# Performance work log

Measured on AMD Instinct MI355X. Metric: run time of the kernel, lower is better.

## Reference

```python
import jax, jax.numpy as jnp
import numpy as np

SQ, B, H = 2048, 1, 4096
NP, HN, MQG = 32, 128, 2          # query heads, head_dim, kv groups
ROT = HN // 2                      # rotary dim = 64 (partial rotary)
NORM = float(np.sqrt(HN))


def apply_rope(x, rope):
    # x: [sq, b, nh, hn]; rope: [sq, 1, ROT//2, 2] (cos, sin)
    sq, b, nh, hn = x.shape
    rot = rope.shape[-2] * 2
    xr, xp = x[..., :rot], x[..., rot:]
    xs = xr.reshape(sq, b, nh, rot // 2, 2)
    rc = rope[:sq].reshape(sq, -1, 1, rot // 2, 2)
    o0 = xs[..., 0] * rc[..., 0] - xs[..., 1] * rc[..., 1]
    o1 = xs[..., 1] * rc[..., 0] + xs[..., 0] * rc[..., 1]
    out = jnp.stack([o0, o1], -1).reshape(sq, b, nh, rot)
    return jnp.concatenate([out, xp], axis=-1)


def setup_inputs() -> dict:
    key = jax.random.key(0)
    k0, k1, k2, k3 = jax.random.split(key, 4)
    qkv_dim = NP * HN + 2 * MQG * HN  # 4608
    hidden_states = jax.random.normal(k0, (SQ, B, H), jnp.float32) * 0.02
    Wqkv = jax.random.normal(k1, (qkv_dim, H), jnp.float32) * 0.02
    bqkv = jax.random.normal(k2, (qkv_dim,), jnp.float32) * 0.02
    Wdense = jax.random.normal(k3, (H, NP * HN), jnp.float32) * 0.02
    # rope cache [sq, 1, ROT//2, 2]
    pos = jnp.arange(SQ, dtype=jnp.float32)
    inv = 1.0 / (10000.0 ** (jnp.arange(0, ROT, 2, dtype=jnp.float32) / ROT))
    ang = pos[:, None] * inv[None, :]
    rotary_pos_emb = jnp.stack([jnp.cos(ang), jnp.sin(ang)], -1)[:, None, :, :]
    # additive causal mask [b, 1, sq, sq]
    causal = jnp.tril(jnp.ones((SQ, SQ), bool))
    attention_mask = jnp.broadcast_to(
        jnp.where(causal, 0.0, -1e9).astype(jnp.float32), (B, 1, SQ, SQ))
    return dict(hidden_states=hidden_states, Wqkv=Wqkv, bqkv=bqkv,
                Wdense=Wdense, rotary_pos_emb=rotary_pos_emb,
                attention_mask=attention_mask)


def reference(hidden_states, Wqkv, bqkv, Wdense, rotary_pos_emb, attention_mask):
    sq, b, _ = hidden_states.shape
    mixed = hidden_states @ Wqkv.T + bqkv            # [sq, b, 4608]
    qd, kvd = NP * HN, MQG * HN
    q = mixed[..., :qd].reshape(sq, b, NP, HN)
    k = mixed[..., qd:qd + kvd].reshape(sq, b, MQG, HN)
    v = mixed[..., qd + kvd:].reshape(sq, b, MQG, HN)
    q = apply_rope(q, rotary_pos_emb)
    k = apply_rope(k, rotary_pos_emb)
    # -> [b, heads, sq, hn]
    q = q.transpose(1, 2, 0, 3)
    k = k.transpose(1, 2, 0, 3)
    v = v.transpose(1, 2, 0, 3)
    # MQA grouping: q [b, g, n_rep, sq, hn]; kv kept at [b, g, sq, hn]
    n_rep = NP // MQG
    qg = q.reshape(b, MQG, n_rep, sq, HN)
    scores = jnp.einsum('bgrqd,bgkd->bgrqk', qg, k) / NORM
    scores = scores + attention_mask[:, None]        # [b,1,1,sq,sq] broadcast
    probs = jax.nn.softmax(scores.astype(jnp.float32), axis=-1).astype(q.dtype)
    ctx = jnp.einsum('bgrqk,bgkd->bgrqd', probs, v)  # [b, g, n_rep, sq, hn]
    ctx = ctx.reshape(b, NP, sq, HN).transpose(0, 2, 1, 3).reshape(b, sq, NP * HN)
    out = ctx @ Wdense.T                             # [b, sq, H]
    return out
```

## Files before the change

kernel.cpp:

```cpp
#include <hip/hip_runtime.h>
#include <stdint.h>

#define SQL 2048
#define HID 4096
#define NHEADS 32
#define HDSZ 128
#define QKVD 4608
#define QDIM 4096

typedef unsigned short u16;
typedef __attribute__((ext_vector_type(8))) short short8;
typedef __attribute__((ext_vector_type(4))) float f32x4;

#define AS1(p) ((__attribute__((address_space(1))) void*)(p))
#define AS3(p) ((__attribute__((address_space(3))) void*)(p))

__device__ __forceinline__ float bf2f(u16 u) {
  return __uint_as_float(((uint32_t)u) << 16);
}
__device__ __forceinline__ u16 f2bf(float f) {
  uint32_t x = __float_as_uint(f);
  x += 0x7fffu + ((x >> 16) & 1u);
  return (u16)(x >> 16);
}

__global__ void k_cvt(const float* __restrict__ in, u16* __restrict__ out, int n8) {
  int i = blockIdx.x * blockDim.x + threadIdx.x;
  int stride = gridDim.x * blockDim.x;
  for (; i < n8; i += stride) {
    const float4* p = reinterpret_cast<const float4*>(in) + (size_t)i * 2;
    float4 a = p[0], b = p[1];
    short8 o;
    o[0] = (short)f2bf(a.x); o[1] = (short)f2bf(a.y);
    o[2] = (short)f2bf(a.z); o[3] = (short)f2bf(a.w);
    o[4] = (short)f2bf(b.x); o[5] = (short)f2bf(b.y);
    o[6] = (short)f2bf(b.z); o[7] = (short)f2bf(b.w);
    reinterpret_cast<short8*>(out)[i] = o;
  }
}

template<int MODE>
__global__ __launch_bounds__(256, 2)
void k_gemm(const u16* __restrict__ A, const u16* __restrict__ B,
            const float* __restrict__ bias,
            u16* __restrict__ qbuf, u16* __restrict__ kbuf, u16* __restrict__ vtbuf,
            float* __restrict__ outf)
{
  __shared__ __align__(16) u16 ldsA[128 * 64];
  __shared__ __align__(16) u16 ldsB[128 * 64];
  const int tid = threadIdx.x;
  const int wid = tid >> 6, lane = tid & 63;
  const int l15 = lane & 15, lg = lane >> 4;
  const int m0 = blockIdx.y * 128, n0 = blockIdx.x * 128;
  const int wr = wid >> 1, wc = wid & 1;

  f32x4 acc[4][4] = {};

  const int srow = lane >> 3;
  const int skb  = (((lane & 7) ^ srow) << 4);
  const size_t rowbytes = (size_t)HID * 2;

  for (int t = 0; t < HID / 64; ++t) {
    __syncthreads();
    const char* Ab = (const char*)A + (size_t)m0 * rowbytes + (size_t)t * 128;
    const char* Bb = (const char*)B + (size_t)n0 * rowbytes + (size_t)t * 128;
#pragma unroll
    for (int i = 0; i < 4; ++i) {
      int seg = i * 4 + wid;
      int row = seg * 8 + srow;
      __builtin_amdgcn_global_load_lds(AS1(Ab + (size_t)row * rowbytes + skb),
                                       AS3(ldsA + seg * 512), 16, 0, 0);
      __builtin_amdgcn_global_load_lds(AS1(Bb + (size_t)row * rowbytes + skb),
                                       AS3(ldsB + seg * 512), 16, 0, 0);
    }
    __syncthreads();
#pragma unroll
    for (int kc = 0; kc < 2; ++kc) {
      short8 af[4], bfr[4];
#pragma unroll
      for (int mi = 0; mi < 4; ++mi) {
        int row = wr * 64 + mi * 16 + l15;
        int kb = (kc * 64 + lg * 16) ^ ((row & 7) << 4);
        af[mi] = *reinterpret_cast<const short8*>((const char*)ldsA + row * 128 + kb);
      }
#pragma unroll
      for (int ni = 0; ni < 4; ++ni) {
        int row = wc * 64 + ni * 16 + l15;
        int kb = (kc * 64 + lg * 16) ^ ((row & 7) << 4);
        bfr[ni] = *reinterpret_cast<const short8*>((const char*)ldsB + row * 128 + kb);
      }
#pragma unroll
      for (int mi = 0; mi < 4; ++mi)
#pragma unroll
        for (int ni = 0; ni < 4; ++ni)
          acc[mi][ni] = __builtin_amdgcn_mfma_f32_16x16x32_bf16(af[mi], bfr[ni], acc[mi][ni], 0, 0, 0);
    }
  }

#pragma unroll
  for (int mi = 0; mi < 4; ++mi) {
#pragma unroll
    for (int ni = 0; ni < 4; ++ni) {
      int row0 = m0 + wr * 64 + mi * 16 + lg * 4;
      int col  = n0 + wc * 64 + ni * 16 + l15;
      if (MODE == 0) {
        float bv = bias[col];
#pragma unroll
        for (int j = 0; j < 4; ++j) {
          float v = acc[mi][ni][j] + bv;
          u16 hb = f2bf(v);
          int r = row0 + j;
          if (col < QDIM) {
            int hh = col >> 7, d = col & 127;
            qbuf[((size_t)hh * SQL + r) * HDSZ + d] = hb;
          } else if (col < QDIM + 256) {
            int c2 = col - QDIM; int g = c2 >> 7, d = c2 & 127;
            kbuf[((size_t)g * SQL + r) * HDSZ + d] = hb;
          } else {
            int c2 = col - QDIM - 256; int g = c2 >> 7, d = c2 & 127;
            vtbuf[((size_t)g * HDSZ + d) * SQL + r] = hb;
          }
        }
      } else {
#pragma unroll
        for (int j = 0; j < 4; ++j)
          outf[(size_t)(row0 + j) * QDIM + col] = acc[mi][ni][j];
      }
    }
  }
}

__global__ void k_rope(u16* __restrict__ qbuf, u16* __restrict__ kbuf,
                       const float* __restrict__ rope) {
  int idx = blockIdx.x * blockDim.x + threadIdx.x;
  if (idx >= SQL * 34 * 32) return;
  int p = idx & 31;
  int hh = (idx >> 5) % 34;
  int s = idx / (34 * 32);
  float c  = rope[s * 64 + p * 2 + 0];
  float sn = rope[s * 64 + p * 2 + 1];
  u16* base = (hh < 32) ? (qbuf + ((size_t)hh * SQL + s) * HDSZ)
                        : (kbuf + ((size_t)(hh - 32) * SQL + s) * HDSZ);
  u16* pp = base + 2 * p;
  uint32_t packed = *reinterpret_cast<uint32_t*>(pp);
  float x0 = bf2f((u16)(packed & 0xffff));
  float x1 = bf2f((u16)(packed >> 16));
  float o0 = x0 * c - x1 * sn;
  float o1 = x1 * c + x0 * sn;
  *reinterpret_cast<uint32_t*>(pp) = (uint32_t)f2bf(o0) | ((uint32_t)f2bf(o1) << 16);
}

__global__ __launch_bounds__(64)
void k_attn(const u16* __restrict__ qbuf, const u16* __restrict__ kbuf,
            const u16* __restrict__ vtbuf, u16* __restrict__ ctx)
{
  __shared__ __align__(16) u16 pls[32 * 72];
  const int lane = threadIdx.x;
  const int l15 = lane & 15, lg = lane >> 4;
  const int h = blockIdx.x;
  const int g = h >> 4;
  const int qi = (int)gridDim.y - 1 - (int)blockIdx.y;
  const int q0 = qi * 32;
  const float inv_norm = 0.08838834764831845f;

  short8 aq[2][4];
#pragma unroll
  for (int rt = 0; rt < 2; ++rt) {
    const u16* qp = qbuf + ((size_t)h * SQL + q0 + rt * 16 + l15) * HDSZ + lg * 8;
#pragma unroll
    for (int kc = 0; kc < 4; ++kc)
      aq[rt][kc] = *reinterpret_cast<const short8*>(qp + kc * 32);
  }
  f32x4 o[2][8] = {};
  float mrow[2][4], lrow[2][4];
#pragma unroll
  for (int rt = 0; rt < 2; ++rt)
#pragma unroll
    for (int j = 0; j < 4; ++j) { mrow[rt][j] = -__builtin_inff(); lrow[rt][j] = 0.f; }

  const int jend = q0 + 31;
  for (int j0 = 0; j0 <= jend; j0 += 64) {
    short8 bk[4][4];
    const u16* kp = kbuf + ((size_t)g * SQL + j0 + l15) * HDSZ + lg * 8;
#pragma unroll
    for (int kt = 0; kt < 4; ++kt)
#pragma unroll
      for (int kc = 0; kc < 4; ++kc)
        bk[kt][kc] = *reinterpret_cast<const short8*>(kp + (size_t)kt * 16 * HDSZ + kc * 32);

    f32x4 s[2][4] = {};
    __builtin_amdgcn_s_setprio(1);
#pragma unroll
    for (int kc = 0; kc < 4; ++kc)
#pragma unroll
      for (int rt = 0; rt < 2; ++rt)
#pragma unroll
        for (int kt = 0; kt < 4; ++kt)
          s[rt][kt] = __builtin_amdgcn_mfma_f32_16x16x32_bf16(aq[rt][kc], bk[kt][kc], s[rt][kt], 0, 0, 0);
    __builtin_amdgcn_s_setprio(0);

    short8 bv[8][2];
    const u16* vp = vtbuf + ((size_t)g * HDSZ + l15) * SQL + j0 + lg * 8;
#pragma unroll
    for (int df = 0; df < 8; ++df)
#pragma unroll
      for (int kc2 = 0; kc2 < 2; ++kc2)
        bv[df][kc2] = *reinterpret_cast<const short8*>(vp + (size_t)df * 16 * SQL + kc2 * 32);

    float al[2][4];
#pragma unroll
    for (int rt = 0; rt < 2; ++rt) {
#pragma unroll
      for (int j = 0; j < 4; ++j) {
        int row = q0 + rt * 16 + lg * 4 + j;
        float v[4];
#pragma unroll
        for (int kt = 0; kt < 4; ++kt) {
          float sv = s[rt][kt][j] * inv_norm;
          v[kt] = (j0 + kt * 16 + l15 > row) ? -1e30f : sv;
        }
        float rm = fmaxf(fmaxf(v[0], v[1]), fmaxf(v[2], v[3]));
        rm = fmaxf(rm, __shfl_xor(rm, 1));
        rm = fmaxf(rm, __shfl_xor(rm, 2));
        rm = fmaxf(rm, __shfl_xor(rm, 4));
        rm = fmaxf(rm, __shfl_xor(rm, 8));
        float mn = fmaxf(mrow[rt][j], rm);
        float a = __expf(mrow[rt][j] - mn);
        mrow[rt][j] = mn;
        float p[4], ps = 0.f;
#pragma unroll
        for (int kt = 0; kt < 4; ++kt) { p[kt] = __expf(v[kt] - mn); ps += p[kt]; }
        ps += __shfl_xor(ps, 1);
        ps += __shfl_xor(ps, 2);
        ps += __shfl_xor(ps, 4);
        ps += __shfl_xor(ps, 8);
        lrow[rt][j] = lrow[rt][j] * a + ps;
        al[rt][j] = a;
        int rl = rt * 16 + lg * 4 + j;
#pragma unroll
        for (int kt = 0; kt < 4; ++kt)
          pls[rl * 72 + kt * 16 + l15] = f2bf(p[kt]);
      }
    }
    asm volatile("s_waitcnt lgkmcnt(0)" ::: "memory");

    short8 ap[2][2];
#pragma unroll
    for (int rt = 0; rt < 2; ++rt)
#pragma unroll
      for (int kc2 = 0; kc2 < 2; ++kc2)
        ap[rt][kc2] = *reinterpret_cast<const short8*>(&pls[(rt * 16 + l15) * 72 + kc2 * 32 + lg * 8]);

    __builtin_amdgcn_s_setprio(1);
#pragma unroll
    for (int rt = 0; rt < 2; ++rt) {
#pragma unroll
      for (int df = 0; df < 8; ++df) {
        f32x4 t = o[rt][df];
        t[0] *= al[rt][0]; t[1] *= al[rt][1]; t[2] *= al[rt][2]; t[3] *= al[rt][3];
        t = __builtin_amdgcn_mfma_f32_16x16x32_bf16(ap[rt][0], bv[df][0], t, 0, 0, 0);
        t = __builtin_amdgcn_mfma_f32_16x16x32_bf16(ap[rt][1], bv[df][1], t, 0, 0, 0);
        o[rt][df] = t;
      }
    }
    __builtin_amdgcn_s_setprio(0);
  }

#pragma unroll
  for (int rt = 0; rt < 2; ++rt) {
#pragma unroll
    for (int j = 0; j < 4; ++j) {
      float inv_l = 1.0f / lrow[rt][j];
      int row = q0 + rt * 16 + lg * 4 + j;
      u16* cp = ctx + (size_t)row * QDIM + h * HDSZ;
#pragma unroll
      for (int df = 0; df < 8; ++df)
        cp[df * 16 + l15] = f2bf(o[rt][df][j] * inv_l);
    }
  }
}


extern "C" void kernel_launch(void* const* d_in, const int* in_sizes, int n_in,
                              void* d_out, int out_size, void* d_ws, size_t ws_size,
                              hipStream_t stream) {
  const float* hs     = (const float*)d_in[0];
  const float* wqkv   = (const float*)d_in[1];
  const float* bqkv   = (const float*)d_in[2];
  const float* wdense = (const float*)d_in[3];
  const float* rope   = (const float*)d_in[4];
  char* ws = (char*)d_ws;
  u16* hid_b = (u16*)(ws + 0);
  u16* w_b   = (u16*)(ws + 16777216);
  u16* qb    = (u16*)(ws + 54525952);
  u16* kb    = (u16*)(ws + 71303168);
  u16* vtb   = (u16*)(ws + 72351744);
  u16* ctx   = hid_b;
  float* outf = (float*)d_out;

  k_cvt<<<2048, 256, 0, stream>>>(hs,   hid_b, SQL * HID / 8);
  k_cvt<<<2048, 256, 0, stream>>>(wqkv, w_b,   QKVD * HID / 8);
  k_gemm<0><<<dim3(QKVD / 128, SQL / 128), 256, 0, stream>>>(
      hid_b, w_b, bqkv, qb, kb, vtb, nullptr);
  k_rope<<<(SQL * 34 * 32) / 256, 256, 0, stream>>>(qb, kb, rope);
  k_cvt<<<2048, 256, 0, stream>>>(wdense, w_b, QDIM * HID / 8);
  k_attn<<<dim3(NHEADS, SQL / 32), 64, 0, stream>>>(qb, kb, vtb, ctx);
  k_gemm<1><<<dim3(QDIM / 128, SQL / 128), 256, 0, stream>>>(
      ctx, w_b, nullptr, nullptr, nullptr, nullptr, outf);
}
```

Before: 338.4 us.

## Split long causal attention rows across two KV chunks with a merge kernel

```diff
diff --git a/kernel.cpp b/kernel.cpp
--- a/kernel.cpp
+++ b/kernel.cpp
@@ -150,17 +150,32 @@
   *reinterpret_cast<uint32_t*>(pp) = (uint32_t)f2bf(o0) | ((uint32_t)f2bf(o1) << 16);
 }
 
+template<int SPLIT>
 __global__ __launch_bounds__(64)
 void k_attn(const u16* __restrict__ qbuf, const u16* __restrict__ kbuf,
-            const u16* __restrict__ vtbuf, u16* __restrict__ ctx)
+            const u16* __restrict__ vtbuf,
+            u16* __restrict__ part, float2* __restrict__ mlbuf,
+            u16* __restrict__ ctx)
 {
   __shared__ __align__(16) u16 pls[32 * 72];
   const int lane = threadIdx.x;
   const int l15 = lane & 15, lg = lane >> 4;
   const int h = blockIdx.x;
   const int g = h >> 4;
-  const int qi = (int)gridDim.y - 1 - (int)blockIdx.y;
+  int qi, ci;
+  if (SPLIT) {
+    int p = blockIdx.y;
+    if (p < 32)      { qi = 32 + p;  ci = 0; }
+    else if (p < 64) { qi = 95 - p;  ci = 1; }
+    else             { qi = 95 - p;  ci = 0; }
+  } else {
+    qi = (int)gridDim.y - 1 - (int)blockIdx.y;
+    ci = 0;
+  }
   const int q0 = qi * 32;
+  const int E  = q0 + 32;
+  const int c0 = SPLIT ? ci * 1024 : 0;
+  const int c1 = SPLIT ? min(c0 + 1024, E) : E;
   const float inv_norm = 0.08838834764831845f;
 
   short8 aq[2][4];
@@ -178,8 +193,7 @@
 #pragma unroll
     for (int j = 0; j < 4; ++j) { mrow[rt][j] = -__builtin_inff(); lrow[rt][j] = 0.f; }
 
-  const int jend = q0 + 31;
-  for (int j0 = 0; j0 <= jend; j0 += 64) {
+  for (int j0 = c0; j0 < c1; j0 += 64) {
     short8 bk[4][4];
     const u16* kp = kbuf + ((size_t)g * SQL + j0 + l15) * HDSZ + lg * 8;
 #pragma unroll
@@ -207,6 +221,7 @@
       for (int kc2 = 0; kc2 < 2; ++kc2)
         bv[df][kc2] = *reinterpret_cast<const short8*>(vp + (size_t)df * 16 * SQL + kc2 * 32);
 
+    const bool domask = (j0 + 63 > q0);
     float al[2][4];
 #pragma unroll
     for (int rt = 0; rt < 2; ++rt) {
@@ -214,10 +229,14 @@
       for (int j = 0; j < 4; ++j) {
         int row = q0 + rt * 16 + lg * 4 + j;
         float v[4];
-#pragma unroll
-        for (int kt = 0; kt < 4; ++kt) {
-          float sv = s[rt][kt][j] * inv_norm;
-          v[kt] = (j0 + kt * 16 + l15 > row) ? -1e30f : sv;
+        if (domask) {
+#pragma unroll
+          for (int kt = 0; kt < 4; ++kt)
+            v[kt] = (j0 + kt * 16 + l15 > row) ? -1e30f : s[rt][kt][j] * inv_norm;
+        } else {
+#pragma unroll
+          for (int kt = 0; kt < 4; ++kt)
+            v[kt] = s[rt][kt][j] * inv_norm;
         }
         float rm = fmaxf(fmaxf(v[0], v[1]), fmaxf(v[2], v[3]));
         rm = fmaxf(rm, __shfl_xor(rm, 1));
@@ -266,20 +285,72 @@
     __builtin_amdgcn_s_setprio(0);
   }
 
-#pragma unroll
-  for (int rt = 0; rt < 2; ++rt) {
-#pragma unroll
-    for (int j = 0; j < 4; ++j) {
-      float inv_l = 1.0f / lrow[rt][j];
-      int row = q0 + rt * 16 + lg * 4 + j;
-      u16* cp = ctx + (size_t)row * QDIM + h * HDSZ;
-#pragma unroll
-      for (int df = 0; df < 8; ++df)
-        cp[df * 16 + l15] = f2bf(o[rt][df][j] * inv_l);
-    }
-  }
-}
-
+  if (SPLIT) {
+    const int pid = (h * 64 + qi) * 2 + ci;
+    u16* pp = part + (size_t)pid * 32 * 128;
+#pragma unroll
+    for (int rt = 0; rt < 2; ++rt) {
+#pragma unroll
+      for (int j = 0; j < 4; ++j) {
+        float inv_l = 1.0f / lrow[rt][j];
+        int rl = rt * 16 + lg * 4 + j;
+#pragma unroll
+        for (int df = 0; df < 8; ++df)
+          pp[rl * 128 + df * 16 + l15] = f2bf(o[rt][df][j] * inv_l);
+        if (l15 == 0)
+          mlbuf[pid * 32 + rl] = make_float2(mrow[rt][j], lrow[rt][j]);
+      }
+    }
+  } else {
+#pragma unroll
+    for (int rt = 0; rt < 2; ++rt) {
+#pragma unroll
+      for (int j = 0; j < 4; ++j) {
+        float inv_l = 1.0f / lrow[rt][j];
+        int row = q0 + rt * 16 + lg * 4 + j;
+        u16* cp = ctx + (size_t)row * QDIM + h * HDSZ;
+#pragma unroll
+        for (int df = 0; df < 8; ++df)
+          cp[df * 16 + l15] = f2bf(o[rt][df][j] * inv_l);
+      }
+    }
+  }
+}
+
+__global__ __launch_bounds__(256)
+void k_merge(const u16* __restrict__ part, const float2* __restrict__ mlbuf,
+             u16* __restrict__ ctx)
+{
+  int idx = blockIdx.x * 256 + threadIdx.x;
+  int d8  = idx & 15;
+  int row = (idx >> 4) & 2047;
+  int h   = idx >> 15;
+  int qi = row >> 5, rl = row & 31;
+  int pid0 = (h * 64 + qi) * 2;
+  float2 ml0 = mlbuf[pid0 * 32 + rl];
+  short8 p0 = *reinterpret_cast<const short8*>(part + ((size_t)pid0 * 32 + rl) * 128 + d8 * 8);
+  short8 p1 = p0;
+  float w0 = ml0.y, w1 = 0.f;
+  if (qi >= 32) {
+    float2 ml1 = mlbuf[(pid0 + 1) * 32 + rl];
+    p1 = *reinterpret_cast<const short8*>(part + ((size_t)(pid0 + 1) * 32 + rl) * 128 + d8 * 8);
+    float ms = fmaxf(ml0.x, ml1.x);
+    w0 = ml0.y * __expf(ml0.x - ms);
+    w1 = ml1.y * __expf(ml1.x - ms);
+  }
+  float inv_s = 1.0f / (w0 + w1);
+  w0 *= inv_s; w1 *= inv_s;
+  short8 o;
+#pragma unroll
+  for (int e = 0; e < 8; ++e)
+    o[e] = (short)f2bf(w0 * bf2f((u16)p0[e]) + w1 * bf2f((u16)p1[e]));
+  *reinterpret_cast<short8*>(ctx + (size_t)row * QDIM + h * 128 + d8 * 8) = o;
+}
+
+
+#define WS_PART 73400320ull
+#define WS_ML   106954752ull
+#define WS_NEED 108003328ull
 
 extern "C" void kernel_launch(void* const* d_in, const int* in_sizes, int n_in,
                               void* d_out, int out_size, void* d_ws, size_t ws_size,
@@ -295,6 +366,8 @@
   u16* qb    = (u16*)(ws + 54525952);
   u16* kb    = (u16*)(ws + 71303168);
   u16* vtb   = (u16*)(ws + 72351744);
+  u16* part  = (u16*)(ws + WS_PART);
+  float2* ml = (float2*)(ws + WS_ML);
   u16* ctx   = hid_b;
   float* outf = (float*)d_out;
 
@@ -304,7 +377,12 @@
       hid_b, w_b, bqkv, qb, kb, vtb, nullptr);
   k_rope<<<(SQL * 34 * 32) / 256, 256, 0, stream>>>(qb, kb, rope);
   k_cvt<<<2048, 256, 0, stream>>>(wdense, w_b, QDIM * HID / 8);
-  k_attn<<<dim3(NHEADS, SQL / 32), 64, 0, stream>>>(qb, kb, vtb, ctx);
+  if (ws_size >= WS_NEED) {
+    k_attn<1><<<dim3(NHEADS, 96), 64, 0, stream>>>(qb, kb, vtb, part, ml, nullptr);
+    k_merge<<<(NHEADS * SQL * 16) / 256, 256, 0, stream>>>(part, ml, ctx);
+  } else {
+    k_attn<0><<<dim3(NHEADS, SQL / 32), 64, 0, stream>>>(qb, kb, vtb, nullptr, nullptr, ctx);
+  }
   k_gemm<1><<<dim3(QDIM / 128, SQL / 128), 256, 0, stream>>>(
       ctx, w_b, nullptr, nullptr, nullptr, nullptr, outf);
 }
```

Result: slower. 369.7 us (+9.3%).

## Transpose score MFMA, fold softmax scale into Q, and add lazy rescaling

Applied to the files above, without the earlier changes.

```diff
diff --git a/kernel.cpp b/kernel.cpp
--- a/kernel.cpp
+++ b/kernel.cpp
@@ -108,17 +108,17 @@
 #pragma unroll
         for (int j = 0; j < 4; ++j) {
           float v = acc[mi][ni][j] + bv;
-          u16 hb = f2bf(v);
           int r = row0 + j;
           if (col < QDIM) {
+            v *= 0.08838834764831845f;
             int hh = col >> 7, d = col & 127;
-            qbuf[((size_t)hh * SQL + r) * HDSZ + d] = hb;
+            qbuf[((size_t)hh * SQL + r) * HDSZ + d] = f2bf(v);
           } else if (col < QDIM + 256) {
             int c2 = col - QDIM; int g = c2 >> 7, d = c2 & 127;
-            kbuf[((size_t)g * SQL + r) * HDSZ + d] = hb;
+            kbuf[((size_t)g * SQL + r) * HDSZ + d] = f2bf(v);
           } else {
             int c2 = col - QDIM - 256; int g = c2 >> 7, d = c2 & 127;
-            vtbuf[((size_t)g * HDSZ + d) * SQL + r] = hb;
+            vtbuf[((size_t)g * HDSZ + d) * SQL + r] = f2bf(v);
           }
         }
       } else {
@@ -154,14 +154,13 @@
 void k_attn(const u16* __restrict__ qbuf, const u16* __restrict__ kbuf,
             const u16* __restrict__ vtbuf, u16* __restrict__ ctx)
 {
-  __shared__ __align__(16) u16 pls[32 * 72];
+  __shared__ uint32_t plw[32][36];
   const int lane = threadIdx.x;
   const int l15 = lane & 15, lg = lane >> 4;
   const int h = blockIdx.x;
   const int g = h >> 4;
   const int qi = (int)gridDim.y - 1 - (int)blockIdx.y;
   const int q0 = qi * 32;
-  const float inv_norm = 0.08838834764831845f;
 
   short8 aq[2][4];
 #pragma unroll
@@ -172,11 +171,9 @@
       aq[rt][kc] = *reinterpret_cast<const short8*>(qp + kc * 32);
   }
   f32x4 o[2][8] = {};
-  float mrow[2][4], lrow[2][4];
-#pragma unroll
-  for (int rt = 0; rt < 2; ++rt)
-#pragma unroll
-    for (int j = 0; j < 4; ++j) { mrow[rt][j] = -__builtin_inff(); lrow[rt][j] = 0.f; }
+  float mrow[2], lrow[2];
+#pragma unroll
+  for (int rt = 0; rt < 2; ++rt) { mrow[rt] = -__builtin_inff(); lrow[rt] = 0.f; }
 
   const int jend = q0 + 31;
   for (int j0 = 0; j0 <= jend; j0 += 64) {
@@ -188,7 +185,7 @@
       for (int kc = 0; kc < 4; ++kc)
         bk[kt][kc] = *reinterpret_cast<const short8*>(kp + (size_t)kt * 16 * HDSZ + kc * 32);
 
-    f32x4 s[2][4] = {};
+    f32x4 st[2][4] = {};
     __builtin_amdgcn_s_setprio(1);
 #pragma unroll
     for (int kc = 0; kc < 4; ++kc)
@@ -196,7 +193,7 @@
       for (int rt = 0; rt < 2; ++rt)
 #pragma unroll
         for (int kt = 0; kt < 4; ++kt)
-          s[rt][kt] = __builtin_amdgcn_mfma_f32_16x16x32_bf16(aq[rt][kc], bk[kt][kc], s[rt][kt], 0, 0, 0);
+          st[rt][kt] = __builtin_amdgcn_mfma_f32_16x16x32_bf16(bk[kt][kc], aq[rt][kc], st[rt][kt], 0, 0, 0);
     __builtin_amdgcn_s_setprio(0);
 
     short8 bv[8][2];
@@ -207,40 +204,62 @@
       for (int kc2 = 0; kc2 < 2; ++kc2)
         bv[df][kc2] = *reinterpret_cast<const short8*>(vp + (size_t)df * 16 * SQL + kc2 * 32);
 
-    float al[2][4];
+    const bool domask = (j0 + 63 > q0);
 #pragma unroll
     for (int rt = 0; rt < 2; ++rt) {
-#pragma unroll
-      for (int j = 0; j < 4; ++j) {
-        int row = q0 + rt * 16 + lg * 4 + j;
-        float v[4];
-#pragma unroll
-        for (int kt = 0; kt < 4; ++kt) {
-          float sv = s[rt][kt][j] * inv_norm;
-          v[kt] = (j0 + kt * 16 + l15 > row) ? -1e30f : sv;
-        }
-        float rm = fmaxf(fmaxf(v[0], v[1]), fmaxf(v[2], v[3]));
-        rm = fmaxf(rm, __shfl_xor(rm, 1));
-        rm = fmaxf(rm, __shfl_xor(rm, 2));
-        rm = fmaxf(rm, __shfl_xor(rm, 4));
-        rm = fmaxf(rm, __shfl_xor(rm, 8));
-        float mn = fmaxf(mrow[rt][j], rm);
-        float a = __expf(mrow[rt][j] - mn);
-        mrow[rt][j] = mn;
-        float p[4], ps = 0.f;
-#pragma unroll
-        for (int kt = 0; kt < 4; ++kt) { p[kt] = __expf(v[kt] - mn); ps += p[kt]; }
-        ps += __shfl_xor(ps, 1);
-        ps += __shfl_xor(ps, 2);
-        ps += __shfl_xor(ps, 4);
-        ps += __shfl_xor(ps, 8);
-        lrow[rt][j] = lrow[rt][j] * a + ps;
-        al[rt][j] = a;
-        int rl = rt * 16 + lg * 4 + j;
-#pragma unroll
-        for (int kt = 0; kt < 4; ++kt)
-          pls[rl * 72 + kt * 16 + l15] = f2bf(p[kt]);
-      }
+      const int q = q0 + rt * 16 + l15;
+      float p[4][4];
+#pragma unroll
+      for (int kt = 0; kt < 4; ++kt)
+#pragma unroll
+        for (int j = 0; j < 4; ++j) {
+          float v = st[rt][kt][j];
+          if (domask) {
+            int kvi = j0 + kt * 16 + lg * 4 + j;
+            v = (kvi > q) ? -1e30f : v;
+          }
+          p[kt][j] = v;
+        }
+      float rm = fmaxf(fmaxf(fmaxf(p[0][0], p[0][1]), fmaxf(p[0][2], p[0][3])),
+                       fmaxf(fmaxf(p[1][0], p[1][1]), fmaxf(p[1][2], p[1][3])));
+      rm = fmaxf(rm, fmaxf(fmaxf(fmaxf(p[2][0], p[2][1]), fmaxf(p[2][2], p[2][3])),
+                           fmaxf(fmaxf(p[3][0], p[3][1]), fmaxf(p[3][2], p[3][3]))));
+      rm = fmaxf(rm, __shfl_xor(rm, 16));
+      rm = fmaxf(rm, __shfl_xor(rm, 32));
+      if (!__all(rm <= mrow[rt] + 8.0f)) {
+        float mn = fmaxf(mrow[rt], rm);
+        float a = __expf(mrow[rt] - mn);
+        mrow[rt] = mn;
+        lrow[rt] *= a;
+        float ar[4];
+#pragma unroll
+        for (int j = 0; j < 4; ++j) ar[j] = __shfl(a, lg * 4 + j);
+#pragma unroll
+        for (int df = 0; df < 8; ++df) {
+          o[rt][df][0] *= ar[0]; o[rt][df][1] *= ar[1];
+          o[rt][df][2] *= ar[2]; o[rt][df][3] *= ar[3];
+        }
+      }
+      float ps = 0.f;
+#pragma unroll
+      for (int kt = 0; kt < 4; ++kt)
+#pragma unroll
+        for (int j = 0; j < 4; ++j) {
+          p[kt][j] = __expf(p[kt][j] - mrow[rt]);
+          ps += p[kt][j];
+        }
+      ps += __shfl_xor(ps, 16);
+      ps += __shfl_xor(ps, 32);
+      lrow[rt] += ps;
+#pragma unroll
+      for (int kt = 0; kt < 4; ++kt)
+#pragma unroll
+        for (int u = 0; u < 2; ++u) {
+          uint32_t W;
+          asm("v_cvt_pk_bf16_f32 %0, %1, %2"
+              : "=v"(W) : "v"(p[kt][2 * u]), "v"(p[kt][2 * u + 1]));
+          plw[rt * 16 + l15][8 * kt + 2 * lg + u] = W;
+        }
     }
     asm volatile("s_waitcnt lgkmcnt(0)" ::: "memory");
 
@@ -249,7 +268,7 @@
     for (int rt = 0; rt < 2; ++rt)
 #pragma unroll
       for (int kc2 = 0; kc2 < 2; ++kc2)
-        ap[rt][kc2] = *reinterpret_cast<const short8*>(&pls[(rt * 16 + l15) * 72 + kc2 * 32 + lg * 8]);
+        ap[rt][kc2] = *reinterpret_cast<const short8*>(&plw[rt * 16 + l15][16 * kc2 + 4 * lg]);
 
     __builtin_amdgcn_s_setprio(1);
 #pragma unroll
@@ -257,7 +276,6 @@
 #pragma unroll
       for (int df = 0; df < 8; ++df) {
         f32x4 t = o[rt][df];
-        t[0] *= al[rt][0]; t[1] *= al[rt][1]; t[2] *= al[rt][2]; t[3] *= al[rt][3];
         t = __builtin_amdgcn_mfma_f32_16x16x32_bf16(ap[rt][0], bv[df][0], t, 0, 0, 0);
         t = __builtin_amdgcn_mfma_f32_16x16x32_bf16(ap[rt][1], bv[df][1], t, 0, 0, 0);
         o[rt][df] = t;
@@ -268,14 +286,16 @@
 
 #pragma unroll
   for (int rt = 0; rt < 2; ++rt) {
+    float linv[4];
+#pragma unroll
+    for (int j = 0; j < 4; ++j) linv[j] = 1.0f / __shfl(lrow[rt], lg * 4 + j);
 #pragma unroll
     for (int j = 0; j < 4; ++j) {
-      float inv_l = 1.0f / lrow[rt][j];
       int row = q0 + rt * 16 + lg * 4 + j;
       u16* cp = ctx + (size_t)row * QDIM + h * HDSZ;
 #pragma unroll
       for (int df = 0; df < 8; ++df)
-        cp[df * 16 + l15] = f2bf(o[rt][df][j] * inv_l);
+        cp[df * 16 + l15] = f2bf(o[rt][df][j] * linv[j]);
     }
   }
 }
```

After: 335.0 us. Within noise of the previous version (-1.0%).
